# Optimization experiments

Hardware: AMD Instinct MI355X
Metric: run time of the kernel (lower is better)

The kernel has to match this reference:

```python
import jax, jax.numpy as jnp
import numpy as np

B, H, N = 256, 128, 2048

def setup_inputs() -> dict:
    key = jax.random.key(0)
    k1, k2, k3, k4, k5 = jax.random.split(key, 5)
    return {
        "static_hidden": jax.random.normal(k1, (B, H, N), dtype=jnp.float32),
        "dynamic_hidden": jax.random.normal(k2, (B, H, N), dtype=jnp.float32),
        "decoder_hidden": jax.random.normal(k3, (B, H), dtype=jnp.float32),
        "v": jax.random.normal(k4, (1, 1, H), dtype=jnp.float32) * 0.05,
        "W": jax.random.normal(k5, (1, H, 3 * H), dtype=jnp.float32) * 0.05,
    }

def reference(static_hidden, dynamic_hidden, decoder_hidden, v, W):
    # hidden: [B, 3H, N] = concat(static, dynamic, broadcast(decoder))
    dec = jnp.broadcast_to(decoder_hidden[:, :, None], static_hidden.shape)
    hidden = jnp.concatenate((static_hidden, dynamic_hidden, dec), axis=1)
    # W @ hidden: [B, H, N]; tanh; v @ .: [B, 1, N]
    Wh = jnp.tanh(jnp.einsum('hk,bkn->bhn', W[0], hidden))
    scores = jnp.einsum('h,bhn->bn', v[0, 0], Wh)[:, None, :]  # [B,1,N]
    return jax.nn.softmax(scores, axis=2)
```

## Files before the change

kernel.cpp:

```cpp
#include <hip/hip_runtime.h>
#include <cstddef>

#define Bn 256
#define Hd 128
#define Nd 2048
#define K3 384

typedef _Float16 half8 __attribute__((ext_vector_type(8)));
typedef float    float4v __attribute__((ext_vector_type(4)));

#define SFENCE() __builtin_amdgcn_sched_barrier(0)

__device__ __forceinline__ float fast_tanh(float x) {
    return 1.0f - __fdividef(2.0f, __expf(2.0f * x) + 1.0f);
}

__global__ void prep_w16(const float* __restrict__ W, _Float16* __restrict__ Wf) {
    int idx = blockIdx.x * 256 + threadIdx.x;
    int h = idx >> 8, k = idx & 255;
    Wf[idx] = (_Float16)W[h * K3 + k];
}

__global__ void prep_c(const float* __restrict__ W, const float* __restrict__ dec,
                       float* __restrict__ cb) {
    __shared__ float dl[Hd];
    int b = blockIdx.x;
    int h = threadIdx.x;
    dl[h] = dec[b * Hd + h];
    __syncthreads();
    float acc = 0.f;
    #pragma unroll 8
    for (int k = 0; k < Hd; ++k)
        acc = fmaf(W[h * K3 + 256 + k], dl[k], acc);
    cb[b * Hd + h] = acc;
}

__global__ __launch_bounds__(256, 2)
void score_kernel(const float* __restrict__ shp, const float* __restrict__ dhp,
                  const _Float16* __restrict__ Wf, const float* __restrict__ cbp,
                  const float* __restrict__ v, float* __restrict__ out) {
    __shared__ __align__(16) _Float16 xl[128 * 256];
    __shared__ float red[4 * 128];

    const int tid  = threadIdx.x;
    const int w    = __builtin_amdgcn_readfirstlane(tid >> 6);
    const int lane = tid & 63;
    const int qd   = lane >> 4;
    const int ln   = lane & 15;
    const int b    = blockIdx.y;
    const int n0   = blockIdx.x * 128;
    const int h0   = w * 32;

    half8 Af[2][8];
    #pragma unroll
    for (int Mt = 0; Mt < 2; ++Mt) {
        const _Float16* wp = Wf + ((h0 + Mt * 16 + ln) << 8) + qd * 8;
        #pragma unroll
        for (int kt = 0; kt < 8; ++kt)
            Af[Mt][kt] = *reinterpret_cast<const half8*>(wp + kt * 32);
    }

    float4v acc[2][8];
    #pragma unroll
    for (int Mt = 0; Mt < 2; ++Mt) {
        float4v c4 = *reinterpret_cast<const float4v*>(cbp + b * Hd + h0 + Mt * 16 + qd * 4);
        #pragma unroll
        for (int Nt = 0; Nt < 8; ++Nt) acc[Mt][Nt] = c4;
    }

    const int n1  = 2 * lane;
    const int swz = lane & 7;
    const size_t bofs = (size_t)b * (Hd * (size_t)Nd) + n0 + n1;

    {
        const float* src = shp + bofs;
        #pragma unroll
        for (int i = 0; i < 4; ++i) {
            const int kl = i * 32 + w * 8;
            float2 xv[8];
            #pragma unroll
            for (int j = 0; j < 8; ++j)
                xv[j] = *reinterpret_cast<const float2*>(src + (size_t)(kl + j) * Nd);
            half8 e0, e1;
            #pragma unroll
            for (int j = 0; j < 8; ++j) {
                e0[j] = (_Float16)xv[j].x;
                e1[j] = (_Float16)xv[j].y;
            }
            const int p = (kl >> 3) ^ swz;
            *reinterpret_cast<half8*>(&xl[n1 * 256 + p * 8])       = e0;
            *reinterpret_cast<half8*>(&xl[(n1 + 1) * 256 + p * 8]) = e1;
        }
    }
    __syncthreads();

    const int swr = (ln >> 1) & 7;
    const float* dsrc = dhp + bofs;

    #pragma unroll
    for (int hp = 0; hp < 2; ++hp) {
        float2 yv[2][8];
        #pragma unroll
        for (int i2 = 0; i2 < 2; ++i2) {
            const int kl = (2 * hp + i2) * 32 + w * 8;
            #pragma unroll
            for (int j = 0; j < 8; ++j)
                yv[i2][j] = *reinterpret_cast<const float2*>(dsrc + (size_t)(kl + j) * Nd);
        }
        SFENCE();

        #pragma unroll
        for (int kt = 2 * hp; kt < 2 * hp + 2; ++kt) {
            half8 Bf[8];
            const int ckb = kt * 4 + qd;
            #pragma unroll
            for (int Nt = 0; Nt < 8; ++Nt) {
                const int row = Nt * 16 + ln;
                Bf[Nt] = *reinterpret_cast<const half8*>(&xl[row * 256 + ((ckb ^ swr) << 3)]);
            }
            #pragma unroll
            for (int Nt = 0; Nt < 8; ++Nt) {
                acc[0][Nt] = __builtin_amdgcn_mfma_f32_16x16x32_f16(Af[0][kt], Bf[Nt], acc[0][Nt], 0, 0, 0);
                acc[1][Nt] = __builtin_amdgcn_mfma_f32_16x16x32_f16(Af[1][kt], Bf[Nt], acc[1][Nt], 0, 0, 0);
            }
        }
        SFENCE();

        #pragma unroll
        for (int i2 = 0; i2 < 2; ++i2) {
            const int kl = (2 * hp + i2) * 32 + w * 8;
            half8 e0, e1;
            #pragma unroll
            for (int j = 0; j < 8; ++j) {
                e0[j] = (_Float16)yv[i2][j].x;
                e1[j] = (_Float16)yv[i2][j].y;
            }
            const int p = ((128 + kl) >> 3) ^ swz;
            *reinterpret_cast<half8*>(&xl[n1 * 256 + p * 8])       = e0;
            *reinterpret_cast<half8*>(&xl[(n1 + 1) * 256 + p * 8]) = e1;
        }
    }
    __syncthreads();

    #pragma unroll
    for (int kt = 4; kt < 8; ++kt) {
        half8 Bf[8];
        const int ckb = kt * 4 + qd;
        #pragma unroll
        for (int Nt = 0; Nt < 8; ++Nt) {
            const int row = Nt * 16 + ln;
            Bf[Nt] = *reinterpret_cast<const half8*>(&xl[row * 256 + ((ckb ^ swr) << 3)]);
        }
        #pragma unroll
        for (int Nt = 0; Nt < 8; ++Nt) {
            acc[0][Nt] = __builtin_amdgcn_mfma_f32_16x16x32_f16(Af[0][kt], Bf[Nt], acc[0][Nt], 0, 0, 0);
            acc[1][Nt] = __builtin_amdgcn_mfma_f32_16x16x32_f16(Af[1][kt], Bf[Nt], acc[1][Nt], 0, 0, 0);
        }
    }

    float4v v0 = *reinterpret_cast<const float4v*>(v + h0 + qd * 4);
    float4v v1 = *reinterpret_cast<const float4v*>(v + h0 + 16 + qd * 4);
    #pragma unroll
    for (int Nt = 0; Nt < 8; ++Nt) {
        float part = 0.f;
        #pragma unroll
        for (int r = 0; r < 4; ++r) {
            part = fmaf(v0[r], fast_tanh(acc[0][Nt][r]), part);
            part = fmaf(v1[r], fast_tanh(acc[1][Nt][r]), part);
        }
        part += __shfl_xor(part, 16);
        part += __shfl_xor(part, 32);
        if (qd == 0) red[w * 128 + Nt * 16 + ln] = part;
    }
    __syncthreads();
    if (tid < 128) {
        float s = red[tid] + red[128 + tid] + red[256 + tid] + red[384 + tid];
        out[(size_t)b * Nd + n0 + tid] = s;
    }
}

__global__ void softmax_k(float* __restrict__ out) {
    int b = blockIdx.x;
    float* row = out + (size_t)b * Nd;
    int tid = threadIdx.x;

    float loc[8];
    float mx = -3.4e38f;
    #pragma unroll
    for (int i = 0; i < 8; ++i) {
        loc[i] = row[tid + (i << 8)];
        mx = fmaxf(mx, loc[i]);
    }
    #pragma unroll
    for (int off = 32; off > 0; off >>= 1) mx = fmaxf(mx, __shfl_xor(mx, off));
    __shared__ float s4[4];
    if ((tid & 63) == 0) s4[tid >> 6] = mx;
    __syncthreads();
    mx = fmaxf(fmaxf(s4[0], s4[1]), fmaxf(s4[2], s4[3]));

    float sum = 0.f;
    #pragma unroll
    for (int i = 0; i < 8; ++i) {
        loc[i] = __expf(loc[i] - mx);
        sum += loc[i];
    }
    #pragma unroll
    for (int off = 32; off > 0; off >>= 1) sum += __shfl_xor(sum, off);
    __shared__ float s4b[4];
    if ((tid & 63) == 0) s4b[tid >> 6] = sum;
    __syncthreads();
    sum = s4b[0] + s4b[1] + s4b[2] + s4b[3];

    float inv = 1.0f / sum;
    #pragma unroll
    for (int i = 0; i < 8; ++i) row[tid + (i << 8)] = loc[i] * inv;
}

extern "C" void kernel_launch(void* const* d_in, const int* in_sizes, int n_in,
                              void* d_out, int out_size, void* d_ws, size_t ws_size,
                              hipStream_t stream) {
    const float* shp = (const float*)d_in[0];
    const float* dhp = (const float*)d_in[1];
    const float* dec = (const float*)d_in[2];
    const float* v   = (const float*)d_in[3];
    const float* W   = (const float*)d_in[4];
    float* out = (float*)d_out;

    _Float16* Wf = (_Float16*)d_ws;
    float* cbp = (float*)((char*)d_ws + 65536);

    hipLaunchKernelGGL(prep_w16, dim3(128), dim3(256), 0, stream, W, Wf);
    hipLaunchKernelGGL(prep_c,   dim3(Bn),  dim3(Hd),  0, stream, W, dec, cbp);
    hipLaunchKernelGGL(score_kernel, dim3(Nd / 128, Bn), dim3(256), 0, stream,
                       shp, dhp, Wf, cbp, v, out);
    hipLaunchKernelGGL(softmax_k, dim3(Bn), dim3(256), 0, stream, out);
}
```

Before: 515.1 us.

## Make score blocks loop over eight batches and prefetch next static slice

Each score block now processes eight consecutive batches for one 128-column tile, using a 1D grid that is eight times smaller. The W fragments and v are loaded once per block and reused across those batches. The static-hidden slice for the next batch is loaded and written to LDS while the MFMAs on the dynamic half of the current batch run. This targets per-block prologue cost and exposed global-load latency. The trade-off is less parallelism (512 blocks) and a longer serial loop per block, which may leave bandwidth unused if overlap is poor.

```diff
diff --git a/kernel.cpp b/kernel.cpp
--- a/kernel.cpp
+++ b/kernel.cpp
@@ -5,6 +5,7 @@
 #define Hd 128
 #define Nd 2048
 #define K3 384
+#define BPC 8
 
 typedef _Float16 half8 __attribute__((ext_vector_type(8)));
 typedef float    float4v __attribute__((ext_vector_type(4)));
@@ -47,8 +48,9 @@
     const int lane = tid & 63;
     const int qd   = lane >> 4;
     const int ln   = lane & 15;
-    const int b    = blockIdx.y;
-    const int n0   = blockIdx.x * 128;
+    const int bid  = blockIdx.x;
+    const int n0   = (bid & 15) * 128;
+    const int b0   = (bid >> 4) * BPC;
     const int h0   = w * 32;
 
     half8 Af[2][8];
@@ -59,123 +61,157 @@
         for (int kt = 0; kt < 8; ++kt)
             Af[Mt][kt] = *reinterpret_cast<const half8*>(wp + kt * 32);
     }
-
-    float4v acc[2][8];
-    #pragma unroll
-    for (int Mt = 0; Mt < 2; ++Mt) {
-        float4v c4 = *reinterpret_cast<const float4v*>(cbp + b * Hd + h0 + Mt * 16 + qd * 4);
-        #pragma unroll
-        for (int Nt = 0; Nt < 8; ++Nt) acc[Mt][Nt] = c4;
-    }
+    const float4v v0 = *reinterpret_cast<const float4v*>(v + h0 + qd * 4);
+    const float4v v1 = *reinterpret_cast<const float4v*>(v + h0 + 16 + qd * 4);
 
     const int n1  = 2 * lane;
     const int swz = lane & 7;
-    const size_t bofs = (size_t)b * (Hd * (size_t)Nd) + n0 + n1;
-
-    {
-        const float* src = shp + bofs;
-        #pragma unroll
-        for (int i = 0; i < 4; ++i) {
-            const int kl = i * 32 + w * 8;
-            float2 xv[8];
-            #pragma unroll
-            for (int j = 0; j < 8; ++j)
-                xv[j] = *reinterpret_cast<const float2*>(src + (size_t)(kl + j) * Nd);
-            half8 e0, e1;
-            #pragma unroll
-            for (int j = 0; j < 8; ++j) {
-                e0[j] = (_Float16)xv[j].x;
-                e1[j] = (_Float16)xv[j].y;
-            }
-            const int p = (kl >> 3) ^ swz;
-            *reinterpret_cast<half8*>(&xl[n1 * 256 + p * 8])       = e0;
-            *reinterpret_cast<half8*>(&xl[(n1 + 1) * 256 + p * 8]) = e1;
-        }
-    }
-    __syncthreads();
-
     const int swr = (ln >> 1) & 7;
-    const float* dsrc = dhp + bofs;
-
-    #pragma unroll
-    for (int hp = 0; hp < 2; ++hp) {
-        float2 yv[2][8];
-        #pragma unroll
-        for (int i2 = 0; i2 < 2; ++i2) {
-            const int kl = (2 * hp + i2) * 32 + w * 8;
-            #pragma unroll
-            for (int j = 0; j < 8; ++j)
-                yv[i2][j] = *reinterpret_cast<const float2*>(dsrc + (size_t)(kl + j) * Nd);
-        }
-        SFENCE();
-
-        #pragma unroll
-        for (int kt = 2 * hp; kt < 2 * hp + 2; ++kt) {
-            half8 Bf[8];
-            const int ckb = kt * 4 + qd;
-            #pragma unroll
-            for (int Nt = 0; Nt < 8; ++Nt) {
-                const int row = Nt * 16 + ln;
-                Bf[Nt] = *reinterpret_cast<const half8*>(&xl[row * 256 + ((ckb ^ swr) << 3)]);
-            }
-            #pragma unroll
-            for (int Nt = 0; Nt < 8; ++Nt) {
-                acc[0][Nt] = __builtin_amdgcn_mfma_f32_16x16x32_f16(Af[0][kt], Bf[Nt], acc[0][Nt], 0, 0, 0);
-                acc[1][Nt] = __builtin_amdgcn_mfma_f32_16x16x32_f16(Af[1][kt], Bf[Nt], acc[1][Nt], 0, 0, 0);
-            }
-        }
-        SFENCE();
-
-        #pragma unroll
-        for (int i2 = 0; i2 < 2; ++i2) {
-            const int kl = (2 * hp + i2) * 32 + w * 8;
-            half8 e0, e1;
-            #pragma unroll
-            for (int j = 0; j < 8; ++j) {
-                e0[j] = (_Float16)yv[i2][j].x;
-                e1[j] = (_Float16)yv[i2][j].y;
-            }
-            const int p = ((128 + kl) >> 3) ^ swz;
-            *reinterpret_cast<half8*>(&xl[n1 * 256 + p * 8])       = e0;
-            *reinterpret_cast<half8*>(&xl[(n1 + 1) * 256 + p * 8]) = e1;
-        }
-    }
-    __syncthreads();
-
-    #pragma unroll
-    for (int kt = 4; kt < 8; ++kt) {
-        half8 Bf[8];
-        const int ckb = kt * 4 + qd;
+    const size_t bstr = (size_t)Hd * Nd;
+    const float* sbase = shp + (size_t)b0 * bstr + n0 + n1;
+    const float* dbase = dhp + (size_t)b0 * bstr + n0 + n1;
+
+    #pragma unroll
+    for (int i = 0; i < 4; ++i) {
+        const int kl = i * 32 + w * 8;
+        float2 xv[8];
+        #pragma unroll
+        for (int j = 0; j < 8; ++j)
+            xv[j] = *reinterpret_cast<const float2*>(sbase + (size_t)(kl + j) * Nd);
+        half8 e0, e1;
+        #pragma unroll
+        for (int j = 0; j < 8; ++j) {
+            e0[j] = (_Float16)xv[j].x;
+            e1[j] = (_Float16)xv[j].y;
+        }
+        const int p = (kl >> 3) ^ swz;
+        *reinterpret_cast<half8*>(&xl[n1 * 256 + p * 8])       = e0;
+        *reinterpret_cast<half8*>(&xl[(n1 + 1) * 256 + p * 8]) = e1;
+    }
+    float4v c0 = *reinterpret_cast<const float4v*>(cbp + (size_t)b0 * Hd + h0 + qd * 4);
+    float4v c1 = *reinterpret_cast<const float4v*>(cbp + (size_t)b0 * Hd + h0 + 16 + qd * 4);
+    __syncthreads();
+
+    #pragma unroll 1
+    for (int it = 0; it < BPC; ++it) {
+        float4v acc[2][8];
+        #pragma unroll
+        for (int Nt = 0; Nt < 8; ++Nt) { acc[0][Nt] = c0; acc[1][Nt] = c1; }
+
+        const float* dsrc = dbase + (size_t)it * bstr;
+
+        #pragma unroll
+        for (int hp = 0; hp < 2; ++hp) {
+            float2 yv[2][8];
+            #pragma unroll
+            for (int i2 = 0; i2 < 2; ++i2) {
+                const int kl = (2 * hp + i2) * 32 + w * 8;
+                #pragma unroll
+                for (int j = 0; j < 8; ++j)
+                    yv[i2][j] = *reinterpret_cast<const float2*>(dsrc + (size_t)(kl + j) * Nd);
+            }
+            SFENCE();
+            #pragma unroll
+            for (int kt = 2 * hp; kt < 2 * hp + 2; ++kt) {
+                half8 Bf[8];
+                const int ckb = kt * 4 + qd;
+                #pragma unroll
+                for (int Nt = 0; Nt < 8; ++Nt) {
+                    const int row = Nt * 16 + ln;
+                    Bf[Nt] = *reinterpret_cast<const half8*>(&xl[row * 256 + ((ckb ^ swr) << 3)]);
+                }
+                #pragma unroll
+                for (int Nt = 0; Nt < 8; ++Nt) {
+                    acc[0][Nt] = __builtin_amdgcn_mfma_f32_16x16x32_f16(Af[0][kt], Bf[Nt], acc[0][Nt], 0, 0, 0);
+                    acc[1][Nt] = __builtin_amdgcn_mfma_f32_16x16x32_f16(Af[1][kt], Bf[Nt], acc[1][Nt], 0, 0, 0);
+                }
+            }
+            SFENCE();
+            #pragma unroll
+            for (int i2 = 0; i2 < 2; ++i2) {
+                const int kl = (2 * hp + i2) * 32 + w * 8;
+                half8 e0, e1;
+                #pragma unroll
+                for (int j = 0; j < 8; ++j) {
+                    e0[j] = (_Float16)yv[i2][j].x;
+                    e1[j] = (_Float16)yv[i2][j].y;
+                }
+                const int p = ((128 + kl) >> 3) ^ swz;
+                *reinterpret_cast<half8*>(&xl[n1 * 256 + p * 8])       = e0;
+                *reinterpret_cast<half8*>(&xl[(n1 + 1) * 256 + p * 8]) = e1;
+            }
+        }
+        __syncthreads();
+
+        const bool pf = (it + 1 < BPC);
+        const float* snxt = sbase + (size_t)(it + 1) * bstr;
+        #pragma unroll
+        for (int hp = 0; hp < 2; ++hp) {
+            float2 xv[2][8];
+            if (pf) {
+                #pragma unroll
+                for (int i2 = 0; i2 < 2; ++i2) {
+                    const int kl = (2 * hp + i2) * 32 + w * 8;
+                    #pragma unroll
+                    for (int j = 0; j < 8; ++j)
+                        xv[i2][j] = *reinterpret_cast<const float2*>(snxt + (size_t)(kl + j) * Nd);
+                }
+            }
+            SFENCE();
+            #pragma unroll
+            for (int kt = 4 + 2 * hp; kt < 6 + 2 * hp; ++kt) {
+                half8 Bf[8];
+                const int ckb = kt * 4 + qd;
+                #pragma unroll
+                for (int Nt = 0; Nt < 8; ++Nt) {
+                    const int row = Nt * 16 + ln;
+                    Bf[Nt] = *reinterpret_cast<const half8*>(&xl[row * 256 + ((ckb ^ swr) << 3)]);
+                }
+                #pragma unroll
+                for (int Nt = 0; Nt < 8; ++Nt) {
+                    acc[0][Nt] = __builtin_amdgcn_mfma_f32_16x16x32_f16(Af[0][kt], Bf[Nt], acc[0][Nt], 0, 0, 0);
+                    acc[1][Nt] = __builtin_amdgcn_mfma_f32_16x16x32_f16(Af[1][kt], Bf[Nt], acc[1][Nt], 0, 0, 0);
+                }
+            }
+            SFENCE();
+            if (pf) {
+                #pragma unroll
+                for (int i2 = 0; i2 < 2; ++i2) {
+                    const int kl = (2 * hp + i2) * 32 + w * 8;
+                    half8 e0, e1;
+                    #pragma unroll
+                    for (int j = 0; j < 8; ++j) {
+                        e0[j] = (_Float16)xv[i2][j].x;
+                        e1[j] = (_Float16)xv[i2][j].y;
+                    }
+                    const int p = (kl >> 3) ^ swz;
+                    *reinterpret_cast<half8*>(&xl[n1 * 256 + p * 8])       = e0;
+                    *reinterpret_cast<half8*>(&xl[(n1 + 1) * 256 + p * 8]) = e1;
+                }
+            }
+        }
+        if (pf) {
+            c0 = *reinterpret_cast<const float4v*>(cbp + (size_t)(b0 + it + 1) * Hd + h0 + qd * 4);
+            c1 = *reinterpret_cast<const float4v*>(cbp + (size_t)(b0 + it + 1) * Hd + h0 + 16 + qd * 4);
+        }
+
         #pragma unroll
         for (int Nt = 0; Nt < 8; ++Nt) {
-            const int row = Nt * 16 + ln;
-            Bf[Nt] = *reinterpret_cast<const half8*>(&xl[row * 256 + ((ckb ^ swr) << 3)]);
-        }
-        #pragma unroll
-        for (int Nt = 0; Nt < 8; ++Nt) {
-            acc[0][Nt] = __builtin_amdgcn_mfma_f32_16x16x32_f16(Af[0][kt], Bf[Nt], acc[0][Nt], 0, 0, 0);
-            acc[1][Nt] = __builtin_amdgcn_mfma_f32_16x16x32_f16(Af[1][kt], Bf[Nt], acc[1][Nt], 0, 0, 0);
-        }
-    }
-
-    float4v v0 = *reinterpret_cast<const float4v*>(v + h0 + qd * 4);
-    float4v v1 = *reinterpret_cast<const float4v*>(v + h0 + 16 + qd * 4);
-    #pragma unroll
-    for (int Nt = 0; Nt < 8; ++Nt) {
-        float part = 0.f;
-        #pragma unroll
-        for (int r = 0; r < 4; ++r) {
-            part = fmaf(v0[r], fast_tanh(acc[0][Nt][r]), part);
-            part = fmaf(v1[r], fast_tanh(acc[1][Nt][r]), part);
-        }
-        part += __shfl_xor(part, 16);
-        part += __shfl_xor(part, 32);
-        if (qd == 0) red[w * 128 + Nt * 16 + ln] = part;
-    }
-    __syncthreads();
-    if (tid < 128) {
-        float s = red[tid] + red[128 + tid] + red[256 + tid] + red[384 + tid];
-        out[(size_t)b * Nd + n0 + tid] = s;
+            float part = 0.f;
+            #pragma unroll
+            for (int r = 0; r < 4; ++r) {
+                part = fmaf(v0[r], fast_tanh(acc[0][Nt][r]), part);
+                part = fmaf(v1[r], fast_tanh(acc[1][Nt][r]), part);
+            }
+            part += __shfl_xor(part, 16);
+            part += __shfl_xor(part, 32);
+            if (qd == 0) red[w * 128 + Nt * 16 + ln] = part;
+        }
+        __syncthreads();
+        if (tid < 128) {
+            float s = red[tid] + red[128 + tid] + red[256 + tid] + red[384 + tid];
+            out[(size_t)(b0 + it) * Nd + n0 + tid] = s;
+        }
     }
 }
 
@@ -231,7 +267,7 @@
 
     hipLaunchKernelGGL(prep_w16, dim3(128), dim3(256), 0, stream, W, Wf);
     hipLaunchKernelGGL(prep_c,   dim3(Bn),  dim3(Hd),  0, stream, W, dec, cbp);
-    hipLaunchKernelGGL(score_kernel, dim3(Nd / 128, Bn), dim3(256), 0, stream,
+    hipLaunchKernelGGL(score_kernel, dim3(16 * (Bn / BPC)), dim3(256), 0, stream,
                        shp, dhp, Wf, cbp, v, out);
     hipLaunchKernelGGL(softmax_k, dim3(Bn), dim3(256), 0, stream, out);
 }
```

Measured after the change: 534.8 us. 1.04x slower.
